# Optimization experiments

Hardware: AMD Instinct MI355X
Metric: run time of the kernel (lower is better)

## Reference

```python
import jax, jax.numpy as jnp
import numpy as np

NUM_HEADS = 4
NUM_GROUPS = 32
EPS = 1e-5


def setup_inputs() -> dict:
    key = jax.random.key(0)
    k1, k2, k3 = jax.random.split(key, 3)
    C = 256
    x = jax.random.normal(k1, (2, C, 64, 64), dtype=jnp.float32)
    gn_scale = jnp.ones((C,), dtype=jnp.float32)
    gn_bias = jnp.zeros((C,), dtype=jnp.float32)
    # 1x1 convs are plain channel-mixing matmuls; init like torch kaiming-uniform-ish
    w_qkv = jax.random.normal(k2, (3 * C, C), dtype=jnp.float32) * (1.0 / np.sqrt(C))
    w_proj = jax.random.normal(k3, (C, C), dtype=jnp.float32) * (1.0 / np.sqrt(C))
    b_proj = jnp.zeros((C,), dtype=jnp.float32)
    return {"x": x, "gn_scale": gn_scale, "gn_bias": gn_bias,
            "w_qkv": w_qkv, "w_proj": w_proj, "b_proj": b_proj}


def _group_norm(x, scale, bias):
    b, c, h, w = x.shape
    xg = x.reshape(b, NUM_GROUPS, c // NUM_GROUPS, h, w)
    mean = xg.mean(axis=(2, 3, 4), keepdims=True)
    var = xg.var(axis=(2, 3, 4), keepdims=True)
    xn = ((xg - mean) * jax.lax.rsqrt(var + EPS)).reshape(b, c, h, w)
    return xn * scale[:, None, None] + bias[:, None, None]


def reference(x, gn_scale, gn_bias, w_qkv, w_proj, b_proj):
    b, c, h, w = x.shape
    hd = c // NUM_HEADS
    scale = hd ** -0.5
    n = h * w

    hn = _group_norm(x, gn_scale, gn_bias)
    # 1x1 conv == channel matmul: (3c, c) @ (b, c, h*w)
    qkv = jnp.einsum('oc,bcn->bon', w_qkv, hn.reshape(b, c, n))
    qkv = qkv.reshape(b, 3, NUM_HEADS, hd, n)
    q, k, v = qkv[:, 0], qkv[:, 1], qkv[:, 2]  # each (b, H, hd, n)

    # scores: (b, H, n, n); softmax over keys (last axis)
    scores = jnp.einsum('bhdn,bhdm->bhnm', q, k) * scale
    attn = jax.nn.softmax(scores, axis=-1)
    out = jnp.einsum('bhnm,bhdm->bhdn', attn, v)  # (b, H, hd, n)
    out = out.reshape(b, c, h, w)

    proj = jnp.einsum('oc,bcn->bon', w_proj, out.reshape(b, c, n)).reshape(b, c, h, w)
    return proj + b_proj[:, None, None] + x
```

## Files before the change

kernel.cpp:

```cpp
#include <hip/hip_runtime.h>
#include <hip/hip_bf16.h>
#include <math.h>

#define Bdim 2
#define Cdim 256
#define Ndim 4096
#define HEADS 4
#define HDim 64

typedef _Float16 half8 __attribute__((ext_vector_type(8)));
typedef _Float16 half4 __attribute__((ext_vector_type(4)));
typedef float f32x4 __attribute__((ext_vector_type(4)));

static const size_t WS_STATS  = 0;
static const size_t WS_WTPROJ = 256;
static const size_t WS_WHQ    = 65792;
static const size_t WS_HN     = 164096;
static const size_t WS_HNT    = 2261248;
static const size_t WS_QT     = 3309824;
static const size_t WS_KT     = 4358400;
static const size_t WS_VF     = 5406976;

#define QSCALE 0.18033688f
#define SINIT  -8.65617025f

__global__ __launch_bounds__(256) void gn_stats_k(const float* __restrict__ x,
                                                  float* __restrict__ stats) {
    int g = blockIdx.x;
    const float4* p4 = (const float4*)(x + (size_t)g * 32768);
    int tid = threadIdx.x;
    float s = 0.f, ss = 0.f;
#pragma unroll 8
    for (int w = 0; w < 32; w++) {
        float4 v = p4[tid + w * 256];
        s += v.x + v.y + v.z + v.w;
        ss += v.x * v.x + v.y * v.y + v.z * v.z + v.w * v.w;
    }
#pragma unroll
    for (int m = 1; m < 64; m <<= 1) {
        s += __shfl_xor(s, m);
        ss += __shfl_xor(ss, m);
    }
    __shared__ float ws_s[4], ws_ss[4];
    int wid = tid >> 6, lane = tid & 63;
    if (lane == 0) { ws_s[wid] = s; ws_ss[wid] = ss; }
    __syncthreads();
    if (tid == 0) {
        float ts = ws_s[0] + ws_s[1] + ws_s[2] + ws_s[3];
        float tss = ws_ss[0] + ws_ss[1] + ws_ss[2] + ws_ss[3];
        float mean = ts * (1.0f / 32768.0f);
        float var = tss * (1.0f / 32768.0f) - mean * mean;
        stats[2 * g] = mean;
        stats[2 * g + 1] = rsqrtf(var + 1e-5f);
    }
}

__global__ __launch_bounds__(256) void gnT_k(const float* __restrict__ x,
                                             const float* __restrict__ stats,
                                             const float* __restrict__ scale,
                                             const float* __restrict__ bias,
                                             _Float16* __restrict__ hnT) {
    __shared__ float t[64][68];
    const int tid = threadIdx.x;
    const int n0 = blockIdx.x << 6, c0 = blockIdx.y << 6, bz = blockIdx.z;
    const int cr = tid >> 2, q4 = tid & 3;
    const int c = c0 + cr;
    const int g = bz * 32 + (c >> 3);
    const float sc = stats[2 * g + 1] * scale[c];
    const float bi = bias[c] - stats[2 * g] * sc;
    const float* base = x + ((size_t)(bz * 256 + c)) * Ndim + n0;
#pragma unroll
    for (int k = 0; k < 4; k++) {
        int j = k * 4 + q4;
        float4 v = *(const float4*)(base + j * 4);
        v.x = v.x * sc + bi; v.y = v.y * sc + bi; v.z = v.z * sc + bi; v.w = v.w * sc + bi;
        *(float4*)&t[cr][j * 4] = v;
    }
    __syncthreads();
    const int nr = tid >> 2, ch = tid & 3;
    half8 o0, o1;
#pragma unroll
    for (int j = 0; j < 8; j++) o0[j] = (_Float16)t[ch * 16 + j][nr];
#pragma unroll
    for (int j = 0; j < 8; j++) o1[j] = (_Float16)t[ch * 16 + 8 + j][nr];
    _Float16* dst = hnT + ((size_t)bz * Ndim + n0 + nr) * 256 + c0 + ch * 16;
    *(half8*)(dst) = o0;
    *(half8*)(dst + 8) = o1;
}

__global__ __launch_bounds__(256) void wcvt_k(const float* __restrict__ w,
                                              _Float16* __restrict__ wh) {
    int i = blockIdx.x * 256 + threadIdx.x;
    float v = w[i];
    if ((i >> 8) < 256) v *= QSCALE;
    wh[i] = (_Float16)v;
}

__global__ __launch_bounds__(256) void tpose_k(const float* __restrict__ W,
                                               float* __restrict__ WT,
                                               int O, int Cc) {
    __shared__ float t[32][33];
    int c0 = blockIdx.x * 32, o0 = blockIdx.y * 32;
    int tx = threadIdx.x, ty = threadIdx.y;
#pragma unroll
    for (int k = 0; k < 4; k++) {
        int o = o0 + ty + k * 8;
        t[ty + k * 8][tx] = W[(size_t)o * Cc + c0 + tx];
    }
    __syncthreads();
#pragma unroll
    for (int k = 0; k < 4; k++) {
        int c = c0 + ty + k * 8;
        WT[(size_t)c * O + o0 + tx] = t[tx][ty + k * 8];
    }
}

__global__ __launch_bounds__(256) void gemm_qkv16_k(const _Float16* __restrict__ wh,
                                                    const _Float16* __restrict__ hnT,
                                                    _Float16* __restrict__ qT,
                                                    _Float16* __restrict__ kT,
                                                    _Float16* __restrict__ vF) {
    __shared__ __align__(16) char smem[32768];
    const int tid = threadIdx.x, w = tid >> 6, lane = tid & 63;
    const int a = lane >> 4, b_ = lane & 15;
    const int wo = w >> 1, wn = w & 1;
    const int n0 = blockIdx.x << 7, o0 = blockIdx.y << 7, bz = blockIdx.z;

    const int srow = tid >> 1, su = (tid & 1) << 1;
    const _Float16* wg = wh + (size_t)(o0 + srow) * 256 + (su << 3);
    const _Float16* xg = hnT + ((size_t)(bz * Ndim + n0 + srow)) * 256 + (su << 3);
    const int wd0 = srow * 64 + ((su ^ (srow & 3)) << 4);
    const int wd1 = srow * 64 + (((su + 1) ^ (srow & 3)) << 4);

    {
        half8 a0 = *(const half8*)(wg), a1 = *(const half8*)(wg + 8);
        half8 b0 = *(const half8*)(xg), b1 = *(const half8*)(xg + 8);
        *(half8*)(smem + wd0) = a0; *(half8*)(smem + wd1) = a1;
        *(half8*)(smem + 16384 + wd0) = b0; *(half8*)(smem + 16384 + wd1) = b1;
    }
    __syncthreads();

    f32x4 acc[4][4] = {};
    const int fa = (a ^ (b_ & 3)) << 4;
    int arow[4], brow[4];
#pragma unroll
    for (int t = 0; t < 4; t++) {
        arow[t] = (wo * 64 + t * 16 + b_) * 64 + fa;
        brow[t] = 16384 + (wn * 64 + t * 16 + b_) * 64 + fa;
    }

    for (int kk = 0; kk < 8; kk++) {
        const int cur = (kk & 1) * 8192;
        half8 nw0, nw1, nx0, nx1;
        const bool pf = (kk < 7);
        if (pf) {
            const _Float16* wp = wg + (kk + 1) * 32;
            const _Float16* xp = xg + (kk + 1) * 32;
            nw0 = *(const half8*)(wp); nw1 = *(const half8*)(wp + 8);
            nx0 = *(const half8*)(xp); nx1 = *(const half8*)(xp + 8);
        }
        half8 af[4], bf[4];
#pragma unroll
        for (int t = 0; t < 4; t++) {
            af[t] = *(const half8*)(smem + cur + arow[t]);
            bf[t] = *(const half8*)(smem + cur + brow[t]);
        }
#pragma unroll
        for (int i = 0; i < 4; i++)
#pragma unroll
            for (int j = 0; j < 4; j++)
                acc[i][j] = __builtin_amdgcn_mfma_f32_16x16x32_f16(af[i], bf[j], acc[i][j], 0, 0, 0);
        if (pf) {
            const int nxt = cur ^ 8192;
            *(half8*)(smem + nxt + wd0) = nw0; *(half8*)(smem + nxt + wd1) = nw1;
            *(half8*)(smem + 16384 + nxt + wd0) = nx0; *(half8*)(smem + 16384 + nxt + wd1) = nx1;
        }
        __syncthreads();
    }

    if (o0 < 512) {
#pragma unroll
        for (int ot = 0; ot < 4; ot++) {
#pragma unroll
            for (int nt = 0; nt < 4; nt++) {
                int n = wn * 64 + nt * 16 + b_;
                int u = wo * 16 + ot * 4 + a;
                half4 hv;
                hv[0] = (_Float16)acc[ot][nt][0]; hv[1] = (_Float16)acc[ot][nt][1];
                hv[2] = (_Float16)acc[ot][nt][2]; hv[3] = (_Float16)acc[ot][nt][3];
                *(half4*)(smem + n * 256 + ((u ^ (n & 31)) << 3)) = hv;
            }
        }
        __syncthreads();
        _Float16* dst = (o0 >= 256) ? kT : qT;
        const int headbase = (o0 >> 6) & 3;
#pragma unroll
        for (int hsel = 0; hsel < 2; hsel++) {
            _Float16* hb = dst + ((size_t)(bz * 4 + headbase + hsel)) * (Ndim * 64);
#pragma unroll
            for (int p = 0; p < 4; p++) {
                int n = p * 32 + (tid >> 3), j = tid & 7;
                int u0 = hsel * 16 + j * 2;
                half4 lo = *(const half4*)(smem + n * 256 + ((u0 ^ (n & 31)) << 3));
                half4 hi = *(const half4*)(smem + n * 256 + (((u0 + 1) ^ (n & 31)) << 3));
                half8 o8;
                o8[0] = lo[0]; o8[1] = lo[1]; o8[2] = lo[2]; o8[3] = lo[3];
                o8[4] = hi[0]; o8[5] = hi[1]; o8[6] = hi[2]; o8[7] = hi[3];
                *(half8*)(hb + (size_t)(n0 + n) * 64 + j * 8) = o8;
            }
        }
    } else {
        _Float16* vb = vF + ((size_t)bz * 256 + (o0 - 512)) * Ndim;
#pragma unroll
        for (int ot = 0; ot < 4; ot++)
#pragma unroll
            for (int nt = 0; nt < 4; nt++)
#pragma unroll
                for (int r = 0; r < 4; r++)
                    vb[(size_t)(wo * 64 + ot * 16 + a * 4 + r) * Ndim +
                       n0 + wn * 64 + nt * 16 + b_] = (_Float16)acc[ot][nt][r];
    }
}

#define LOADKV(S, st)                                                        \
    {                                                                        \
        const _Float16* kp_ = Kp + (size_t)(st) * 2048;                      \
        S##k00 = *(const half8*)(kp_);                                       \
        S##k01 = *(const half8*)(kp_ + 32);                                  \
        S##k10 = *(const half8*)(kp_ + 1024);                                \
        S##k11 = *(const half8*)(kp_ + 1024 + 32);                           \
        const _Float16* vp_ = Vp + (st) * 32;                                \
        _Pragma("unroll") for (int dt = 0; dt < 4; dt++) {                   \
            S##v[dt][0] = *(const half4*)(vp_ + dt * 16 * Ndim);             \
            S##v[dt][1] = *(const half4*)(vp_ + dt * 16 * Ndim + 16);        \
        }                                                                    \
    }

#define COMPUTE(S)                                                                        \
    {                                                                                     \
        _Pragma("unroll") for (int qi = 0; qi < 4; qi++) {                                \
            f32x4 s0 = {SINIT, SINIT, SINIT, SINIT}, s1 = s0;                             \
            s0 = __builtin_amdgcn_mfma_f32_16x16x32_f16(S##k00, qf0[qi], s0, 0, 0, 0);    \
            s0 = __builtin_amdgcn_mfma_f32_16x16x32_f16(S##k01, qf1[qi], s0, 0, 0, 0);    \
            s1 = __builtin_amdgcn_mfma_f32_16x16x32_f16(S##k10, qf0[qi], s1, 0, 0, 0);    \
            s1 = __builtin_amdgcn_mfma_f32_16x16x32_f16(S##k11, qf1[qi], s1, 0, 0, 0);    \
            half4 alo, ahi;                                                               \
            float rs = 0.f;                                                               \
            _Pragma("unroll") for (int r = 0; r < 4; r++) {                               \
                float e0 = __builtin_exp2f(s0[r]);                                        \
                float e1 = __builtin_exp2f(s1[r]);                                        \
                rs += e0 + e1;                                                            \
                alo[r] = (_Float16)e0;                                                    \
                ahi[r] = (_Float16)e1;                                                    \
            }                                                                             \
            lr[qi] += rs;                                                                 \
            _Pragma("unroll") for (int dt = 0; dt < 4; dt++) {                            \
                oa[qi][dt] = __builtin_amdgcn_mfma_f32_16x16x16f16(alo, S##v[dt][0],      \
                                                                   oa[qi][dt], 0, 0, 0); \
                oa[qi][dt] = __builtin_amdgcn_mfma_f32_16x16x16f16(ahi, S##v[dt][1],      \
                                                                   oa[qi][dt], 0, 0, 0); \
            }                                                                             \
        }                                                                                 \
    }

__global__ __launch_bounds__(256, 2) void attn_k(const _Float16* __restrict__ qT,
                                                 const _Float16* __restrict__ kT,
                                                 const _Float16* __restrict__ vF,
                                                 float* __restrict__ outp) {
    __shared__ __align__(16) char smem[33792];
    const int tid = threadIdx.x;
    const int w = tid >> 6, lane = tid & 63;
    const int a = lane >> 4, b_ = lane & 15;
    const int s = blockIdx.x;
    const int o = ((s & 7) << 6) + (s >> 3);
    const int qt = o & 63;
    const size_t bh = (size_t)(o >> 6);
    const int q0 = qt << 6;
    const _Float16* Qb = qT + bh * (size_t)(Ndim * 64);
    const _Float16* Kb = kT + bh * (size_t)(Ndim * 64);
    const _Float16* Vb = vF + bh * (size_t)(64 * Ndim);

    half8 qf0[4], qf1[4];
#pragma unroll
    for (int qi = 0; qi < 4; qi++) {
        const _Float16* qp = Qb + (size_t)(q0 + qi * 16 + b_) * 64 + a * 8;
        qf0[qi] = *(const half8*)(qp);
        qf1[qi] = *(const half8*)(qp + 32);
    }

    const int kb = w << 10;
    const _Float16* Kp = Kb + (size_t)(kb + b_) * 64 + a * 8;
    const _Float16* Vp = Vb + (size_t)b_ * Ndim + kb + a * 4;

    f32x4 oa[4][4] = {};
    float lr[4] = {0.f, 0.f, 0.f, 0.f};

    half8 Ak00, Ak01, Ak10, Ak11; half4 Av[4][2];
    half8 Bk00, Bk01, Bk10, Bk11; half4 Bv[4][2];

    LOADKV(A, 0);
    for (int st = 0; st < 32; st += 2) {
        LOADKV(B, st + 1);
        COMPUTE(A);
        if (st + 2 < 32) LOADKV(A, st + 2);
        COMPUTE(B);
    }

    float lrw[4];
#pragma unroll
    for (int qi = 0; qi < 4; qi++) {
        float t = lr[qi];
        t += __shfl_xor(t, 16);
        t += __shfl_xor(t, 32);
        lrw[qi] = t;
    }
    float* lrs = (float*)(smem + 32768);
    if (a == 0) {
#pragma unroll
        for (int qi = 0; qi < 4; qi++) lrs[w * 64 + qi * 16 + b_] = lrw[qi];
    }

    float* Ow = (float*)(smem + ((w & 1) << 14));
    if (w < 2) {
#pragma unroll
        for (int qi = 0; qi < 4; qi++)
#pragma unroll
            for (int dt = 0; dt < 4; dt++) {
                int off = (16 * dt + b_) * 64 + (((qi * 4 + a) ^ b_) << 2);
                *(f32x4*)(Ow + off) = oa[qi][dt];
            }
    }
    __syncthreads();
    if (w >= 2) {
#pragma unroll
        for (int qi = 0; qi < 4; qi++)
#pragma unroll
            for (int dt = 0; dt < 4; dt++) {
                int off = (16 * dt + b_) * 64 + (((qi * 4 + a) ^ b_) << 2);
                f32x4 v = *(const f32x4*)(Ow + off);
                v += oa[qi][dt];
                *(f32x4*)(Ow + off) = v;
            }
    }
    __syncthreads();

    {
        const float* R0 = (const float*)(smem);
        const float* R1 = (const float*)(smem + 16384);
        int dr = tid >> 4, qc = tid & 15;
        f32x4 lt = *(const f32x4*)(lrs + qc * 4);
        lt += *(const f32x4*)(lrs + 64 + qc * 4);
        lt += *(const f32x4*)(lrs + 128 + qc * 4);
        lt += *(const f32x4*)(lrs + 192 + qc * 4);
        f32x4 inv;
#pragma unroll
        for (int r = 0; r < 4; r++) inv[r] = 1.0f / lt[r];
#pragma unroll
        for (int p = 0; p < 4; p++) {
            int d = p * 16 + dr;
            int off = d * 64 + ((qc ^ (d & 15)) << 2);
            f32x4 v = *(const f32x4*)(R0 + off);
            v += *(const f32x4*)(R1 + off);
#pragma unroll
            for (int r = 0; r < 4; r++) v[r] *= inv[r];
            *(f32x4*)(outp + (bh * 64 + d) * (size_t)Ndim + q0 + (qc << 2)) = v;
        }
    }
}

__global__ __launch_bounds__(256) void gemm_proj_k(const float* __restrict__ WT,
                                                   const float* __restrict__ X,
                                                   float* __restrict__ out,
                                                   const float* __restrict__ bias,
                                                   const float* __restrict__ resid) {
    __shared__ __align__(16) float Ws[32][128];
    __shared__ __align__(16) float Xs[32][128];
    const int tid = threadIdx.x, tx = tid & 15, ty = tid >> 4;
    const int n0 = blockIdx.x << 7, o0 = blockIdx.y << 7;
    const size_t bX = (size_t)blockIdx.z * Cdim * Ndim;
    float acc[8][8] = {};
    for (int k0 = 0; k0 < Cdim; k0 += 32) {
        __syncthreads();
#pragma unroll
        for (int kq = 0; kq < 4; kq++) {
            int f4 = tid + (kq << 8);
            int r = f4 >> 5, cc = (f4 & 31) << 2;
            *(float4*)&Ws[r][cc] = *(const float4*)(WT + (size_t)(k0 + r) * 256 + o0 + cc);
            *(float4*)&Xs[r][cc] = *(const float4*)(X + bX + (size_t)(k0 + r) * Ndim + n0 + cc);
        }
        __syncthreads();
#pragma unroll 4
        for (int kk = 0; kk < 32; kk++) {
            float4 wa = *(const float4*)&Ws[kk][ty << 2];
            float4 wb = *(const float4*)&Ws[kk][(ty << 2) + 64];
            float4 xa = *(const float4*)&Xs[kk][tx << 2];
            float4 xb = *(const float4*)&Xs[kk][(tx << 2) + 64];
            float wv[8] = {wa.x, wa.y, wa.z, wa.w, wb.x, wb.y, wb.z, wb.w};
            float xv[8] = {xa.x, xa.y, xa.z, xa.w, xb.x, xb.y, xb.z, xb.w};
#pragma unroll
            for (int i = 0; i < 8; i++)
#pragma unroll
                for (int j = 0; j < 8; j++)
                    acc[i][j] = fmaf(wv[i], xv[j], acc[i][j]);
        }
    }
#pragma unroll
    for (int i = 0; i < 8; i++) {
        int o = o0 + (ty << 2) + ((i < 4) ? i : (64 + i - 4));
        size_t rowoff = bX + (size_t)o * Ndim + n0 + (tx << 2);
        float bv = bias[o];
        float4 r0, r1;
        r0.x = acc[i][0] + bv; r0.y = acc[i][1] + bv; r0.z = acc[i][2] + bv; r0.w = acc[i][3] + bv;
        r1.x = acc[i][4] + bv; r1.y = acc[i][5] + bv; r1.z = acc[i][6] + bv; r1.w = acc[i][7] + bv;
        float4 x0 = *(const float4*)(resid + rowoff);
        float4 x1 = *(const float4*)(resid + rowoff + 64);
        r0.x += x0.x; r0.y += x0.y; r0.z += x0.z; r0.w += x0.w;
        r1.x += x1.x; r1.y += x1.y; r1.z += x1.z; r1.w += x1.w;
        *(float4*)(out + rowoff) = r0;
        *(float4*)(out + rowoff + 64) = r1;
    }
}

extern "C" void kernel_launch(void* const* d_in, const int* in_sizes, int n_in,
                              void* d_out, int out_size, void* d_ws, size_t ws_size,
                              hipStream_t stream) {
    (void)in_sizes; (void)n_in; (void)out_size; (void)ws_size;
    const float* x        = (const float*)d_in[0];
    const float* gn_scale = (const float*)d_in[1];
    const float* gn_bias  = (const float*)d_in[2];
    const float* w_qkv    = (const float*)d_in[3];
    const float* w_proj   = (const float*)d_in[4];
    const float* b_proj   = (const float*)d_in[5];
    float* ws    = (float*)d_ws;
    float* stats = ws + WS_STATS;
    float* wtp   = ws + WS_WTPROJ;
    _Float16* whq = (_Float16*)(ws + WS_WHQ);
    float* hn    = ws + WS_HN;
    _Float16* hnT = (_Float16*)(ws + WS_HNT);
    _Float16* qT = (_Float16*)(ws + WS_QT);
    _Float16* kT = (_Float16*)(ws + WS_KT);
    _Float16* vF = (_Float16*)(ws + WS_VF);
    float* outp  = (float*)d_out;

    gn_stats_k<<<64, 256, 0, stream>>>(x, stats);
    gnT_k<<<dim3(64, 4, 2), 256, 0, stream>>>(x, stats, gn_scale, gn_bias, hnT);
    wcvt_k<<<768, 256, 0, stream>>>(w_qkv, whq);
    tpose_k<<<dim3(8, 8), dim3(32, 8), 0, stream>>>(w_proj, wtp, 256, 256);
    gemm_qkv16_k<<<dim3(32, 6, 2), 256, 0, stream>>>(whq, hnT, qT, kT, vF);
    attn_k<<<512, 256, 0, stream>>>(qT, kT, vF, hn);
    gemm_proj_k<<<dim3(32, 2, 2), 256, 0, stream>>>(wtp, hn, outp, b_proj, x);
}
```

Measured before the change: 231.9 us.

## Pack K and V into MFMA-fragment order so attention loads are contiguous

The QKV GEMM epilogue now writes K and V into a packed layout that matches the per-lane MFMA fragment order used by the attention kernel. Each wave's K/V loads per step become contiguous 1 KB (K) and coalesced half4 chunks (V) instead of strided row reads across Ndim. This targets memory coalescing in the attention inner loop. In exchange the GEMM epilogue does more scattered stores for V (2-byte stores at strided offsets).

```diff
diff --git a/kernel.cpp b/kernel.cpp
--- a/kernel.cpp
+++ b/kernel.cpp
@@ -18,8 +18,8 @@
 static const size_t WS_HN     = 164096;
 static const size_t WS_HNT    = 2261248;
 static const size_t WS_QT     = 3309824;
-static const size_t WS_KT     = 4358400;
-static const size_t WS_VF     = 5406976;
+static const size_t WS_KPK    = 4358400;
+static const size_t WS_VPK    = 5406976;
 
 #define QSCALE 0.18033688f
 #define SINIT  -8.65617025f
@@ -118,8 +118,8 @@
 __global__ __launch_bounds__(256) void gemm_qkv16_k(const _Float16* __restrict__ wh,
                                                     const _Float16* __restrict__ hnT,
                                                     _Float16* __restrict__ qT,
-                                                    _Float16* __restrict__ kT,
-                                                    _Float16* __restrict__ vF) {
+                                                    _Float16* __restrict__ kpk,
+                                                    _Float16* __restrict__ vpk) {
     __shared__ __align__(16) char smem[32768];
     const int tid = threadIdx.x, w = tid >> 6, lane = tid & 63;
     const int a = lane >> 4, b_ = lane & 15;
@@ -192,11 +192,11 @@
             }
         }
         __syncthreads();
-        _Float16* dst = (o0 >= 256) ? kT : qT;
         const int headbase = (o0 >> 6) & 3;
+        const bool isq = (o0 < 256);
 #pragma unroll
         for (int hsel = 0; hsel < 2; hsel++) {
-            _Float16* hb = dst + ((size_t)(bz * 4 + headbase + hsel)) * (Ndim * 64);
+            const int bhh = bz * 4 + headbase + hsel;
 #pragma unroll
             for (int p = 0; p < 4; p++) {
                 int n = p * 32 + (tid >> 3), j = tid & 7;
@@ -206,19 +206,34 @@
                 half8 o8;
                 o8[0] = lo[0]; o8[1] = lo[1]; o8[2] = lo[2]; o8[3] = lo[3];
                 o8[4] = hi[0]; o8[5] = hi[1]; o8[6] = hi[2]; o8[7] = hi[3];
-                *(half8*)(hb + (size_t)(n0 + n) * 64 + j * 8) = o8;
+                int n_g = n0 + n;
+                if (isq) {
+                    *(half8*)(qT + (size_t)bhh * (Ndim * 64) + (size_t)n_g * 64 + j * 8) = o8;
+                } else {
+                    int sg = n_g >> 5, nm = n_g & 31;
+                    int f = ((nm >> 4) << 1) | (j >> 2);
+                    int off = sg * 2048 + f * 512 + (((j & 3) << 4) | (nm & 15)) * 8;
+                    *(half8*)(kpk + (size_t)bhh * 262144 + off) = o8;
+                }
             }
         }
     } else {
-        _Float16* vb = vF + ((size_t)bz * 256 + (o0 - 512)) * Ndim;
-#pragma unroll
-        for (int ot = 0; ot < 4; ot++)
-#pragma unroll
-            for (int nt = 0; nt < 4; nt++)
+        const int rowbase = (o0 - 512) + wo * 64;
+        const int hh = rowbase >> 6;
+        _Float16* vb = vpk + (size_t)(bz * 4 + hh) * 262144;
+        const int i_ = b_ & 3, aslot = b_ >> 2;
+#pragma unroll
+        for (int ot = 0; ot < 4; ot++) {
+#pragma unroll
+            for (int nt = 0; nt < 4; nt++) {
+                int n_g = n0 + wn * 64 + nt * 16;
+                int sg = n_g >> 5, sub = (n_g >> 4) & 1;
+                int base = sg * 2048 + (ot * 2 + sub) * 256 + (aslot << 6) + i_;
 #pragma unroll
                 for (int r = 0; r < 4; r++)
-                    vb[(size_t)(wo * 64 + ot * 16 + a * 4 + r) * Ndim +
-                       n0 + wn * 64 + nt * 16 + b_] = (_Float16)acc[ot][nt][r];
+                    vb[base + (a * 4 + r) * 4] = (_Float16)acc[ot][nt][r];
+            }
+        }
     }
 }
 
@@ -226,13 +241,13 @@
     {                                                                        \
         const _Float16* kp_ = Kp + (size_t)(st) * 2048;                      \
         S##k00 = *(const half8*)(kp_);                                       \
-        S##k01 = *(const half8*)(kp_ + 32);                                  \
+        S##k01 = *(const half8*)(kp_ + 512);                                 \
         S##k10 = *(const half8*)(kp_ + 1024);                                \
-        S##k11 = *(const half8*)(kp_ + 1024 + 32);                           \
-        const _Float16* vp_ = Vp + (st) * 32;                                \
+        S##k11 = *(const half8*)(kp_ + 1536);                                \
+        const _Float16* vp_ = Vp + (size_t)(st) * 2048;                      \
         _Pragma("unroll") for (int dt = 0; dt < 4; dt++) {                   \
-            S##v[dt][0] = *(const half4*)(vp_ + dt * 16 * Ndim);             \
-            S##v[dt][1] = *(const half4*)(vp_ + dt * 16 * Ndim + 16);        \
+            S##v[dt][0] = *(const half4*)(vp_ + (dt * 2 + 0) * 256);         \
+            S##v[dt][1] = *(const half4*)(vp_ + (dt * 2 + 1) * 256);         \
         }                                                                    \
     }
 
@@ -264,8 +279,8 @@
     }
 
 __global__ __launch_bounds__(256, 2) void attn_k(const _Float16* __restrict__ qT,
-                                                 const _Float16* __restrict__ kT,
-                                                 const _Float16* __restrict__ vF,
+                                                 const _Float16* __restrict__ kpk,
+                                                 const _Float16* __restrict__ vpk,
                                                  float* __restrict__ outp) {
     __shared__ __align__(16) char smem[33792];
     const int tid = threadIdx.x;
@@ -277,8 +292,6 @@
     const size_t bh = (size_t)(o >> 6);
     const int q0 = qt << 6;
     const _Float16* Qb = qT + bh * (size_t)(Ndim * 64);
-    const _Float16* Kb = kT + bh * (size_t)(Ndim * 64);
-    const _Float16* Vb = vF + bh * (size_t)(64 * Ndim);
 
     half8 qf0[4], qf1[4];
 #pragma unroll
@@ -288,9 +301,8 @@
         qf1[qi] = *(const half8*)(qp + 32);
     }
 
-    const int kb = w << 10;
-    const _Float16* Kp = Kb + (size_t)(kb + b_) * 64 + a * 8;
-    const _Float16* Vp = Vb + (size_t)b_ * Ndim + kb + a * 4;
+    const _Float16* Kp = kpk + bh * 262144 + (size_t)(w * 32) * 2048 + (size_t)lane * 8;
+    const _Float16* Vp = vpk + bh * 262144 + (size_t)(w * 32) * 2048 + (size_t)lane * 4;
 
     f32x4 oa[4][4] = {};
     float lr[4] = {0.f, 0.f, 0.f, 0.f};
@@ -438,15 +450,15 @@
     float* hn    = ws + WS_HN;
     _Float16* hnT = (_Float16*)(ws + WS_HNT);
     _Float16* qT = (_Float16*)(ws + WS_QT);
-    _Float16* kT = (_Float16*)(ws + WS_KT);
-    _Float16* vF = (_Float16*)(ws + WS_VF);
+    _Float16* kpk = (_Float16*)(ws + WS_KPK);
+    _Float16* vpk = (_Float16*)(ws + WS_VPK);
     float* outp  = (float*)d_out;
 
     gn_stats_k<<<64, 256, 0, stream>>>(x, stats);
     gnT_k<<<dim3(64, 4, 2), 256, 0, stream>>>(x, stats, gn_scale, gn_bias, hnT);
     wcvt_k<<<768, 256, 0, stream>>>(w_qkv, whq);
     tpose_k<<<dim3(8, 8), dim3(32, 8), 0, stream>>>(w_proj, wtp, 256, 256);
-    gemm_qkv16_k<<<dim3(32, 6, 2), 256, 0, stream>>>(whq, hnT, qT, kT, vF);
-    attn_k<<<512, 256, 0, stream>>>(qT, kT, vF, hn);
+    gemm_qkv16_k<<<dim3(32, 6, 2), 256, 0, stream>>>(whq, hnT, qT, kpk, vpk);
+    attn_k<<<512, 256, 0, stream>>>(qT, kpk, vpk, hn);
     gemm_proj_k<<<dim3(32, 2, 2), 256, 0, stream>>>(wtp, hn, outp, b_proj, x);
 }
```

New measurement: 193.8 us. 1.2x faster.
